# Kernel tuning notes

Measured on AMD Instinct MI355X. Metric: run time of the kernel, lower is better.

The kernel has to match this reference:

```python
import jax, jax.numpy as jnp
import numpy as np

BATCH = 8
NDATA = 8192
NPOINT = 1024
NSAMPLE = 32
RADIUS = 0.2
CFEAT = 64


def setup_inputs() -> dict:
    key = jax.random.key(0)
    k1, k2, k3 = jax.random.split(key, 3)
    new_xyz = jax.random.normal(k1, (BATCH, NPOINT, 3), dtype=jnp.float32)
    xyz = jax.random.normal(k2, (BATCH, NDATA, 3), dtype=jnp.float32)
    points = jax.random.normal(k3, (BATCH, NDATA, CFEAT), dtype=jnp.float32)
    return {"new_xyz": new_xyz, "xyz": xyz, "points": points}


def reference(new_xyz, xyz, points):
    # Pairwise distances from every centroid to every dataset point.
    # delta: [B, P, N, 3]
    delta = xyz[:, None, :, :] - new_xyz[:, :, None, :]
    dist = jnp.linalg.norm(delta, axis=-1)  # [B, P, N]

    # Sort by distance (the original does a full argsort per centroid).
    sorted_idx = jnp.argsort(dist, axis=-1).astype(jnp.int32)  # [B, P, N]
    sorted_d = jnp.take_along_axis(dist, sorted_idx, axis=-1)  # [B, P, N]

    # Nearest point index replaces out-of-radius slots.
    nearest = sorted_idx[:, :, 0:1]  # [B, P, 1]
    radius_idx = jnp.where(sorted_d < RADIUS, sorted_idx, nearest)
    idx = radius_idx[:, :, :NSAMPLE]  # [B, P, S] int32 (ndataset >= nsample)

    # Batched gathers: grouped_xyz [B, P, S, 3], grouped_points [B, P, S, C].
    grouped_xyz = jnp.take_along_axis(
        xyz[:, None, :, :], idx[..., None], axis=2)
    grouped_points = jnp.take_along_axis(
        points[:, None, :, :], idx[..., None], axis=2)
    new_points = jnp.concatenate([grouped_xyz, grouped_points], axis=-1)
    return (new_points, idx, grouped_xyz)
```

## Files before the change

### kernel.cpp

```cpp
#include <hip/hip_runtime.h>
#include <math.h>

typedef unsigned int   u32;
typedef unsigned long long u64;

#define BATCH   8
#define NDATA   8192
#define NPOINT  1024
#define NSAMPLE 32
#define CFEAT   64
#define ROWF    67
#define MAXCAND 128
#define QPB     4
#define NB      256

#define OUT_IDX (BATCH*NPOINT*NSAMPLE*ROWF)
#define OUT_GX  (OUT_IDX + BATCH*NPOINT*NSAMPLE)

__device__ __forceinline__ float rnbf(float f) {
    u32 b = __float_as_uint(f);
    b += 0x7FFFu + ((b >> 16) & 1u);
    return __uint_as_float(b & 0xFFFF0000u);
}
__device__ __forceinline__ int clampidx(int v) {
    return (v < 0) ? 0 : (v > NDATA-1 ? NDATA-1 : v);
}
__device__ __forceinline__ int xbucket(float v) {
    int c = (int)floorf((v + 4.5f) * 28.444445f);
    return c < 0 ? 0 : (c > NB-1 ? NB-1 : c);
}

__global__ __launch_bounds__(1024)
void bin_kernel(const float* __restrict__ xyz,
                float4* __restrict__ wp, u32* __restrict__ wst)
{
    __shared__ u32 cnt[NB];
    __shared__ u32 sc[NB];
    const int b = blockIdx.x, tid = threadIdx.x;
    const float* bx = xyz + (size_t)b * NDATA * 3;

    if (tid < NB) cnt[tid] = 0;
    __syncthreads();
    for (int p = tid; p < NDATA; p += 1024)
        atomicAdd(&cnt[xbucket(bx[p*3])], 1u);
    __syncthreads();

    if (tid < NB) sc[tid] = cnt[tid];
    __syncthreads();
    #pragma unroll
    for (int d = 1; d < NB; d <<= 1) {
        u32 t = 0;
        if (tid < NB && tid >= d) t = sc[tid - d];
        __syncthreads();
        if (tid < NB && tid >= d) sc[tid] += t;
        __syncthreads();
    }
    if (tid < NB) {
        u32 excl = (tid == 0) ? 0u : sc[tid - 1];
        cnt[tid] = excl;
        wst[b*(NB+1) + tid] = excl;
        if (tid == 0) wst[b*(NB+1) + NB] = NDATA;
    }
    __syncthreads();

    for (int p = tid; p < NDATA; p += 1024) {
        float x = bx[p*3], y = bx[p*3+1], z = bx[p*3+2];
        u32 pos = atomicAdd(&cnt[xbucket(x)], 1u);
        wp[(size_t)b*NDATA + pos] = make_float4(x, y, z, __uint_as_float((u32)p));
    }
}

__global__ __launch_bounds__(256, 8)
void grouping_kernel(const float* __restrict__ new_xyz,
                     const float* __restrict__ xyz,
                     const float* __restrict__ points,
                     const float4* __restrict__ wp, const u32* __restrict__ wst,
                     float* __restrict__ out, float T)
{
    __shared__ float cand_s[QPB][MAXCAND];
    __shared__ int   cand_i[QPB][MAXCAND];
    __shared__ int   sel[QPB][NSAMPLE];

    const int tid  = threadIdx.x;
    const int wv   = tid >> 6;
    const int lane = tid & 63;
    const int q    = blockIdx.x * QPB + wv;
    const int b    = q >> 10;

    if (lane < NSAMPLE) sel[wv][lane] = 0;

    const float qx = new_xyz[q*3 + 0];
    const float qy = new_xyz[q*3 + 1];
    const float qz = new_xyz[q*3 + 2];
    const float*  bx = xyz + (size_t)b * NDATA * 3;
    const float4* cp = wp  + (size_t)b * NDATA;

    const int blo = xbucket(__fsub_rn(qx, 0.2005f));
    const int bhi = xbucket(__fadd_rn(qx, 0.2005f));
    const u32 j0 = wst[b*(NB+1) + blo];
    const u32 j1 = wst[b*(NB+1) + bhi + 1];

    int n = 0;
    for (u32 jb = j0; jb < j1; jb += 64) {
        u32 j  = jb + lane;
        bool in = j < j1;
        u32 jj = in ? j : (j1 - 1);
        float4 v = cp[jj];
        float dx = __fsub_rn(v.x, qx);
        float dy = __fsub_rn(v.y, qy);
        float dz = __fsub_rn(v.z, qz);
        float d2 = __fadd_rn(__fadd_rn(__fmul_rn(dx,dx), __fmul_rn(dy,dy)),
                             __fmul_rn(dz,dz));
        bool cc = in && (d2 < T);
        u64 m = __ballot(cc);
        if (m) {
            if (cc) {
                int below = __builtin_amdgcn_mbcnt_hi((u32)(m >> 32),
                             __builtin_amdgcn_mbcnt_lo((u32)m, 0));
                int pos = n + below;
                if (pos < MAXCAND) {
                    cand_s[wv][pos] = __fsqrt_rn(d2);
                    cand_i[wv][pos] = (int)__float_as_uint(v.w);
                }
            }
            n += (int)__popcll(m);
        }
    }

    int mini = 0;
    if (n == 0) {
        float mind = 3.402823466e38f; int mi = 0;
        for (int k = 0; k < NDATA/64; ++k) {
            int i = (k << 6) + lane;
            float dx = __fsub_rn(bx[i*3+0], qx);
            float dy = __fsub_rn(bx[i*3+1], qy);
            float dz = __fsub_rn(bx[i*3+2], qz);
            float d2 = __fadd_rn(__fadd_rn(__fmul_rn(dx,dx), __fmul_rn(dy,dy)),
                                 __fmul_rn(dz,dz));
            if (d2 < mind) { mind = d2; mi = i; }
        }
        float ms = __fsqrt_rn(mind);
        for (int off = 32; off; off >>= 1) {
            float os = __shfl_xor(ms, off);
            int   oi = __shfl_xor(mi, off);
            if (os < ms || (os == ms && oi < mi)) { ms = os; mi = oi; }
        }
        mini = mi;
    }

    __syncthreads();

    const int nj = n > MAXCAND ? MAXCAND : n;
    for (int kk = lane; kk < nj; kk += 64) {
        float sk = cand_s[wv][kk];
        int   ik = cand_i[wv][kk];
        int r = 0;
        for (int mm = 0; mm < nj; ++mm) {
            float sm = cand_s[wv][mm];
            int   im = cand_i[wv][mm];
            r += (int)((sm < sk) | ((sm == sk) & (im < ik)));
        }
        if (r < NSAMPLE) sel[wv][r] = clampidx(ik);
    }
    __syncthreads();
    {
        const int nsel = nj < NSAMPLE ? nj : NSAMPLE;
        if (lane >= nsel && lane < NSAMPLE) {
            int pad = (nj > 0) ? sel[wv][0] : clampidx(mini);
            sel[wv][lane] = pad;
        }
    }
    __syncthreads();

    if (lane < NSAMPLE)
        out[OUT_IDX + (size_t)q*NSAMPLE + lane] = rnbf((float)sel[wv][lane]);

    for (int e = lane; e < NSAMPLE*3; e += 64) {
        int sR = e / 3, c2 = e - sR*3;
        int is = sel[wv][sR];
        out[OUT_GX + (size_t)q*(NSAMPLE*3) + e] = rnbf(bx[is*3 + c2]);
    }

    const float* prow = points + (size_t)b * NDATA * CFEAT;
    float* onp = out + (size_t)q * (NSAMPLE*ROWF);
    for (int e = lane; e < NSAMPLE*ROWF; e += 64) {
        int sR = e / ROWF;
        int c2 = e - sR*ROWF;
        int is = sel[wv][sR];
        const float* ap = (c2 < 3) ? (bx + (size_t)is*3 + c2)
                                   : (prow + (size_t)is*CFEAT + (c2-3));
        onp[e] = rnbf(*ap);
    }
}

extern "C" void kernel_launch(void* const* d_in, const int* in_sizes, int n_in,
                              void* d_out, int out_size, void* d_ws, size_t ws_size,
                              hipStream_t stream) {
    union { u32 u; float f; } lo, hi, mid;
    lo.u = 0u; hi.f = 0.05f;
    while (hi.u - lo.u > 1u) {
        mid.u = lo.u + (hi.u - lo.u) / 2u;
        if (sqrtf(mid.f) >= 0.2f) hi.u = mid.u; else lo.u = mid.u;
    }
    float T = hi.f;

    float4* wp  = (float4*)d_ws;
    u32*    wst = (u32*)(wp + (size_t)BATCH*NDATA);

    const float* nxz = (const float*)d_in[0];
    const float* xyz = (const float*)d_in[1];
    const float* pts = (const float*)d_in[2];

    bin_kernel<<<BATCH, 1024, 0, stream>>>(xyz, wp, wst);
    grouping_kernel<<<(BATCH*NPOINT)/QPB, 256, 0, stream>>>(
        nxz, xyz, pts, wp, wst, (float*)d_out, T);
}
```

Before: 131.0 us.

## Split feature gather into separate kernel with one block per query

Moves the large grouped-feature gather out of the grouping kernel into a new gather_kernel launched with one 256-thread block per query. Selected indices are written to a workspace buffer so the second kernel can read them. The aim is more parallelism and better memory-level concurrency on the bandwidth-heavy output write, instead of one wave per query doing the whole copy. The cost is an extra kernel launch and an extra round-trip of the indices through global memory.

```diff
diff --git a/kernel.cpp b/kernel.cpp
--- a/kernel.cpp
+++ b/kernel.cpp
@@ -75,6 +75,7 @@
                      const float* __restrict__ xyz,
                      const float* __restrict__ points,
                      const float4* __restrict__ wp, const u32* __restrict__ wst,
+                     u32* __restrict__ selws,
                      float* __restrict__ out, float T)
 {
     __shared__ float cand_s[QPB][MAXCAND];
@@ -172,21 +173,38 @@
     }
     __syncthreads();
 
-    if (lane < NSAMPLE)
-        out[OUT_IDX + (size_t)q*NSAMPLE + lane] = rnbf((float)sel[wv][lane]);
-
+    if (lane < NSAMPLE) {
+        int v = sel[wv][lane];
+        out[OUT_IDX + (size_t)q*NSAMPLE + lane] = rnbf((float)v);
+        selws[(size_t)q*NSAMPLE + lane] = (u32)v;
+    }
     for (int e = lane; e < NSAMPLE*3; e += 64) {
         int sR = e / 3, c2 = e - sR*3;
         int is = sel[wv][sR];
         out[OUT_GX + (size_t)q*(NSAMPLE*3) + e] = rnbf(bx[is*3 + c2]);
     }
-
+}
+
+__global__ __launch_bounds__(256, 8)
+void gather_kernel(const float* __restrict__ xyz,
+                   const float* __restrict__ points,
+                   const u32* __restrict__ selws,
+                   float* __restrict__ out)
+{
+    __shared__ int ssel[NSAMPLE];
+    const int q = blockIdx.x;
+    const int b = q >> 10;
+    if (threadIdx.x < NSAMPLE)
+        ssel[threadIdx.x] = (int)selws[(size_t)q*NSAMPLE + threadIdx.x];
+    __syncthreads();
+
+    const float* bx   = xyz    + (size_t)b * NDATA * 3;
     const float* prow = points + (size_t)b * NDATA * CFEAT;
     float* onp = out + (size_t)q * (NSAMPLE*ROWF);
-    for (int e = lane; e < NSAMPLE*ROWF; e += 64) {
+    for (int e = threadIdx.x; e < NSAMPLE*ROWF; e += 256) {
         int sR = e / ROWF;
         int c2 = e - sR*ROWF;
-        int is = sel[wv][sR];
+        int is = ssel[sR];
         const float* ap = (c2 < 3) ? (bx + (size_t)is*3 + c2)
                                    : (prow + (size_t)is*CFEAT + (c2-3));
         onp[e] = rnbf(*ap);
@@ -206,6 +224,7 @@
 
     float4* wp  = (float4*)d_ws;
     u32*    wst = (u32*)(wp + (size_t)BATCH*NDATA);
+    u32*    selws = wst + BATCH*(NB+1);
 
     const float* nxz = (const float*)d_in[0];
     const float* xyz = (const float*)d_in[1];
@@ -213,5 +232,6 @@
 
     bin_kernel<<<BATCH, 1024, 0, stream>>>(xyz, wp, wst);
     grouping_kernel<<<(BATCH*NPOINT)/QPB, 256, 0, stream>>>(
-        nxz, xyz, pts, wp, wst, (float*)d_out, T);
-}
+        nxz, xyz, pts, wp, wst, selws, (float*)d_out, T);
+    gather_kernel<<<BATCH*NPOINT, 256, 0, stream>>>(xyz, pts, selws, (float*)d_out);
+}
```

Result: slower. 138.4 us (+5.7%).
